# Kernel tuning notes

Hardware: AMD Instinct MI355X
Metric: run time of the kernel (lower is better)

## Reference

```python
import jax, jax.numpy as jnp
import numpy as np

N_HEADS = 16
N_EMBD = 1024
HEAD_SIZE = N_EMBD // N_HEADS
B, T = 4, 2048
EPS = 1e-5


def _layernorm(x, g, b):
    mu = jnp.mean(x, axis=-1, keepdims=True)
    var = jnp.mean((x - mu) ** 2, axis=-1, keepdims=True)
    return (x - mu) * jax.lax.rsqrt(var + EPS) * g + b


def setup_inputs() -> dict:
    key = jax.random.key(0)
    ks = jax.random.split(key, 12)
    s_in = 1.0 / np.sqrt(N_EMBD)
    s_ff = 1.0 / np.sqrt(4 * N_EMBD)
    return {
        "x": jax.random.normal(ks[0], (B, T, N_EMBD), jnp.float32),
        "Wq": jax.random.normal(ks[1], (N_HEADS, N_EMBD, HEAD_SIZE), jnp.float32) * s_in,
        "Wk": jax.random.normal(ks[2], (N_HEADS, N_EMBD, HEAD_SIZE), jnp.float32) * s_in,
        "Wv": jax.random.normal(ks[3], (N_HEADS, N_EMBD, HEAD_SIZE), jnp.float32) * s_in,
        "Wproj": jax.random.normal(ks[4], (N_EMBD, N_EMBD), jnp.float32) * s_in,
        "bproj": jnp.zeros((N_EMBD,), jnp.float32),
        "ln1_g": jnp.ones((N_EMBD,), jnp.float32),
        "ln1_b": jnp.zeros((N_EMBD,), jnp.float32),
        "ln2_g": jnp.ones((N_EMBD,), jnp.float32),
        "ln2_b": jnp.zeros((N_EMBD,), jnp.float32),
        "W1": jax.random.normal(ks[5], (N_EMBD, 4 * N_EMBD), jnp.float32) * s_in,
        "b1": jnp.zeros((4 * N_EMBD,), jnp.float32),
        "W2": jax.random.normal(ks[6], (4 * N_EMBD, N_EMBD), jnp.float32) * s_ff,
        "b2": jnp.zeros((N_EMBD,), jnp.float32),
    }


def reference(x, Wq, Wk, Wv, Wproj, bproj, ln1_g, ln1_b, ln2_g, ln2_b, W1, b1, W2, b2):
    Bx, Tx, C = x.shape
    # --- self-attention on ln1(x) ---
    h = _layernorm(x, ln1_g, ln1_b)
    q = jnp.einsum('btc,hcd->bhtd', h, Wq)
    k = jnp.einsum('btc,hcd->bhtd', h, Wk)
    v = jnp.einsum('btc,hcd->bhtd', h, Wv)
    # NOTE: original scales by C**-0.5 where C = n_embd (full dim), not head_size
    scores = jnp.einsum('bhtd,bhsd->bhts', q, k) * (C ** -0.5)
    causal = jnp.tril(jnp.ones((Tx, Tx), dtype=bool))
    scores = jnp.where(causal, scores, -jnp.inf)
    wei = jax.nn.softmax(scores, axis=-1)
    attn = jnp.einsum('bhts,bhsd->bhtd', wei, v)  # [B,H,T,hs]
    attn = attn.transpose(0, 2, 1, 3).reshape(Bx, Tx, -1)  # concat heads -> [B,T,C]
    x = x + attn @ Wproj + bproj
    # --- feed-forward on ln2(x) ---
    h2 = _layernorm(x, ln2_g, ln2_b)
    ff = jax.nn.relu(h2 @ W1 + b1) @ W2 + b2
    return x + ff
```

## Files before the change

kernel.cpp:

```cpp
#include <hip/hip_runtime.h>
#include <math.h>

typedef short bf16x8 __attribute__((ext_vector_type(8)));
typedef float f32x4 __attribute__((ext_vector_type(4)));
typedef unsigned short u16;

__device__ __forceinline__ u16 f2bf(float f) {
    union { float f; unsigned u; } v; v.f = f;
    unsigned r = v.u + 0x7fffu + ((v.u >> 16) & 1u);
    return (u16)(r >> 16);
}

__device__ __forceinline__ void gload_lds16(const void* g, void* l) {
    __builtin_amdgcn_global_load_lds((const __attribute__((address_space(1))) void*)g,
                                     (__attribute__((address_space(3))) void*)l, 16, 0, 0);
}

__global__ __launch_bounds__(256)
void transpose_cvt(const float* __restrict__ in, u16* __restrict__ out, int R, int C)
{
    __shared__ float tile[64][65];
    const size_t slab = (size_t)blockIdx.z * R * C;
    const float* ip = in + slab;
    u16* op = out + slab;
    const int r0 = blockIdx.y * 64, c0 = blockIdx.x * 64;
    const int t = threadIdx.x;
    const int tr = t >> 6, tc = t & 63;
    #pragma unroll
    for (int i = 0; i < 16; ++i)
        tile[tr + i*4][tc] = ip[(size_t)(r0 + tr + i*4)*C + c0 + tc];
    __syncthreads();
    #pragma unroll
    for (int i = 0; i < 16; ++i)
        op[(size_t)(c0 + tr + i*4)*R + r0 + tc] = f2bf(tile[tc][tr + i*4]);
}

__global__ __launch_bounds__(256)
void ln_kernel(const float* __restrict__ x, const float* __restrict__ g,
               const float* __restrict__ b, u16* __restrict__ out)
{
    const int row = blockIdx.x;
    const int t = threadIdx.x;
    const float4 v = ((const float4*)(x + (size_t)row*1024))[t];
    float s = v.x + v.y + v.z + v.w;
    float ss = v.x*v.x + v.y*v.y + v.z*v.z + v.w*v.w;
    #pragma unroll
    for (int m = 1; m < 64; m <<= 1) {
        s  += __shfl_xor(s, m);
        ss += __shfl_xor(ss, m);
    }
    __shared__ float red[8];
    const int wave = t >> 6;
    if ((t & 63) == 0) { red[wave] = s; red[4 + wave] = ss; }
    __syncthreads();
    s  = red[0] + red[1] + red[2] + red[3];
    ss = red[4] + red[5] + red[6] + red[7];
    const float mu = s * (1.f/1024.f);
    const float rs = rsqrtf(ss * (1.f/1024.f) - mu*mu + 1e-5f);
    const float4 gv = ((const float4*)g)[t];
    const float4 bv = ((const float4*)b)[t];
    ushort4 ov;
    ov.x = f2bf((v.x - mu)*rs*gv.x + bv.x);
    ov.y = f2bf((v.y - mu)*rs*gv.y + bv.y);
    ov.z = f2bf((v.z - mu)*rs*gv.z + bv.z);
    ov.w = f2bf((v.w - mu)*rs*gv.w + bv.w);
    ((ushort4*)(out + (size_t)row*1024))[t] = ov;
}

template<int NWG, int BN, int N, int K, int EPI>
__global__ __launch_bounds__(512, 2)
void gemm256_kernel(const u16* __restrict__ A, const u16* __restrict__ BT,
                    float* __restrict__ out_f32, u16* __restrict__ out_bf16,
                    const float* __restrict__ bias, const float* __restrict__ res,
                    u16* __restrict__ qbuf, u16* __restrict__ kbuf, u16* __restrict__ vt)
{
    constexpr int NI  = BN / 128;
    constexpr int NCB = BN / 64;
    __shared__ u16 As[2][256*64];
    __shared__ u16 Bs[2][BN*64];

    const int bid = blockIdx.x;
    const int tid = ((bid & 7) * (NWG / 8)) + (bid >> 3);
    const int m0 = (tid & 31) * 256;
    const int n0 = (tid >> 5) * BN;
    const int t = threadIdx.x;
    const int lane = t & 63;
    const int l15 = lane & 15, lg = lane >> 4;
    const int wid = t >> 6;
    const int wm = wid >> 2, wn = wid & 3;
    const int swzf = (l15 & 7) << 4;

    f32x4 acc[2][2][4][NI] = {};
    bf16x8 af[4][2], b0[NI][2], b1[NI][2];

    const int srow = t >> 3;
    const int sg8  = ((t & 7) ^ (srow & 7)) * 8;

#define SA_H(BUF, K0, H) do { \
    _Pragma("unroll") \
    for (int i = 2*(H); i < 2*(H)+2; ++i) \
        gload_lds16(A + (size_t)(m0 + i*64 + srow)*K + (K0) + sg8, &As[BUF][i*4096 + t*8]); \
} while (0)
#define SB_H(BUF, K0, H) do { \
    _Pragma("unroll") \
    for (int i = (NCB/2)*(H); i < (NCB/2)*(H) + NCB/2; ++i) \
        gload_lds16(BT + (size_t)(n0 + i*64 + srow)*K + (K0) + sg8, &Bs[BUF][i*4096 + t*8]); \
} while (0)
#define RD_A(CUR, QM) do { \
    _Pragma("unroll") \
    for (int mi = 0; mi < 4; ++mi) \
        _Pragma("unroll") \
        for (int kk = 0; kk < 2; ++kk) \
            af[mi][kk] = *(const bf16x8*)((const char*)&As[CUR][0] \
                + ((QM)*128 + wm*64 + mi*16 + l15)*128 + ((kk*64 + lg*16) ^ swzf)); \
} while (0)
#define RD_B(CUR, QN, DST) do { \
    _Pragma("unroll") \
    for (int ni = 0; ni < NI; ++ni) \
        _Pragma("unroll") \
        for (int kk = 0; kk < 2; ++kk) \
            DST[ni][kk] = *(const bf16x8*)((const char*)&Bs[CUR][0] \
                + ((QN)*(BN/2) + wn*(BN/8) + ni*16 + l15)*128 + ((kk*64 + lg*16) ^ swzf)); \
} while (0)
#define MFMAQ(QM, QN, BF) do { \
    _Pragma("unroll") \
    for (int mi = 0; mi < 4; ++mi) \
        _Pragma("unroll") \
        for (int ni = 0; ni < NI; ++ni) \
            _Pragma("unroll") \
            for (int kk = 0; kk < 2; ++kk) \
                acc[QM][QN][mi][ni] = __builtin_amdgcn_mfma_f32_16x16x32_bf16( \
                    af[mi][kk], BF[ni][kk], acc[QM][QN][mi][ni], 0, 0, 0); \
} while (0)
#define PH_MFMA(QM, QN, BF) do { \
    __builtin_amdgcn_sched_barrier(0); \
    __builtin_amdgcn_s_barrier(); \
    asm volatile("s_waitcnt lgkmcnt(0)" ::: "memory"); \
    __builtin_amdgcn_sched_barrier(0); \
    __builtin_amdgcn_s_setprio(1); \
    MFMAQ(QM, QN, BF); \
    __builtin_amdgcn_s_setprio(0); \
    __builtin_amdgcn_sched_barrier(0); \
} while (0)
#define BAR __builtin_amdgcn_s_barrier()
#define W_B1S do { if constexpr (BN == 256) asm volatile("s_waitcnt vmcnt(6)":::"memory"); \
                   else                     asm volatile("s_waitcnt vmcnt(5)":::"memory"); } while (0)
#define W_A1S do { if constexpr (BN == 256) asm volatile("s_waitcnt vmcnt(6)":::"memory"); \
                   else                     asm volatile("s_waitcnt vmcnt(4)":::"memory"); } while (0)
#define W_01S do { if constexpr (BN == 256) asm volatile("s_waitcnt vmcnt(4)":::"memory"); \
                   else                     asm volatile("s_waitcnt vmcnt(3)":::"memory"); } while (0)
#define W_B1L asm volatile("s_waitcnt vmcnt(2)":::"memory")
#define W_A1L asm volatile("s_waitcnt vmcnt(0)":::"memory")

    SA_H(0, 0, 0); SB_H(0, 0, 0);
    SB_H(0, 0, 1);
    SA_H(0, 0, 1);
    W_01S; BAR;

    const int NKT = K / 64;
    for (int kt = 0; kt < NKT - 1; ++kt) {
        const int cur = kt & 1, nxt = cur ^ 1;
        const int k1 = (kt + 1) * 64;
        RD_A(cur, 0); RD_B(cur, 0, b0);
        SA_H(nxt, k1, 0); SB_H(nxt, k1, 0);
        PH_MFMA(0, 0, b0);
        W_B1S; BAR;
        RD_B(cur, 1, b1);
        SB_H(nxt, k1, 1);
        PH_MFMA(0, 1, b1);
        W_A1S; BAR;
        RD_A(cur, 1);
        SA_H(nxt, k1, 1);
        PH_MFMA(1, 1, b1);
        BAR;
        PH_MFMA(1, 0, b0);
        W_01S; BAR;
    }
    {
        const int cur = (NKT - 1) & 1;
        RD_A(cur, 0); RD_B(cur, 0, b0);
        PH_MFMA(0, 0, b0);
        W_B1L; BAR;
        RD_B(cur, 1, b1);
        PH_MFMA(0, 1, b1);
        W_A1L; BAR;
        RD_A(cur, 1);
        PH_MFMA(1, 1, b1);
        BAR;
        PH_MFMA(1, 0, b0);
    }
#undef SA_H
#undef SB_H
#undef RD_A
#undef RD_B
#undef MFMAQ
#undef PH_MFMA
#undef BAR
#undef W_B1S
#undef W_A1S
#undef W_01S
#undef W_B1L
#undef W_A1L

    #pragma unroll
    for (int qm = 0; qm < 2; ++qm)
      #pragma unroll
      for (int qn = 0; qn < 2; ++qn)
        #pragma unroll
        for (int mi = 0; mi < 4; ++mi)
          #pragma unroll
          for (int ni = 0; ni < NI; ++ni) {
            const int gc = n0 + qn*(BN/2) + wn*(BN/8) + ni*16 + l15;
            #pragma unroll
            for (int j = 0; j < 4; ++j) {
                const int gr = m0 + qm*128 + wm*64 + mi*16 + lg*4 + j;
                float v = acc[qm][qn][mi][ni][j];
                if constexpr (EPI == 0) {
                    u16 bv = f2bf(v);
                    if (gc < 1024) {
                        qbuf[(size_t)gr*1024 + gc] = bv;
                    } else if (gc < 2048) {
                        kbuf[(size_t)gr*1024 + (gc - 1024)] = bv;
                    } else {
                        const int hd = gc - 2048;
                        const int bb = gr >> 11, tt = gr & 2047;
                        vt[(size_t)((bb*16 + (hd >> 6))*64 + (hd & 63))*2048 + tt] = bv;
                    }
                } else if constexpr (EPI == 1) {
                    out_f32[(size_t)gr*N + gc] = v + bias[gc] + res[(size_t)gr*N + gc];
                } else {
                    out_bf16[(size_t)gr*N + gc] = f2bf(fmaxf(v + bias[gc], 0.f));
                }
            }
          }
}

__device__ __forceinline__ void attn_qtile(
    bf16x8 (&qf)[2][2], f32x4 (&o)[2][4], float (&mprev)[2][4], float (&lsum)[2][4],
    const u16* Ksc, const u16* Vsc, u16* pl,
    int key0, int q0, int l15, int lg, int swzf, int swzp)
{
    #pragma unroll
    for (int mi = 0; mi < 2; ++mi) {
        if (key0 > q0 + mi*16 + 15) continue;
        f32x4 s[4] = {};
        #pragma unroll
        for (int n = 0; n < 4; ++n)
            #pragma unroll
            for (int kk = 0; kk < 2; ++kk) {
                const int row = n*16 + l15;
                bf16x8 kf = *(const bf16x8*)((const char*)Ksc
                                + row*128 + ((kk*64 + lg*16) ^ swzf));
                s[n] = __builtin_amdgcn_mfma_f32_16x16x32_bf16(qf[mi][kk], kf, s[n], 0, 0, 0);
            }
        const bool domask = (key0 + 63) > (q0 + mi*16);
        float tm[4] = {-INFINITY, -INFINITY, -INFINITY, -INFINITY};
        #pragma unroll
        for (int n = 0; n < 4; ++n)
            #pragma unroll
            for (int j = 0; j < 4; ++j) {
                float sv = s[n][j] * 0.03125f;
                if (domask && (key0 + n*16 + l15 > q0 + mi*16 + lg*4 + j)) sv = -INFINITY;
                s[n][j] = sv;
                tm[j] = fmaxf(tm[j], sv);
            }
        #pragma unroll
        for (int m = 1; m < 16; m <<= 1)
            #pragma unroll
            for (int j = 0; j < 4; ++j)
                tm[j] = fmaxf(tm[j], __shfl_xor(tm[j], m, 16));
        float alpha[4], rsum[4];
        #pragma unroll
        for (int j = 0; j < 4; ++j) {
            float mn = fmaxf(mprev[mi][j], tm[j]);
            alpha[j] = __expf(mprev[mi][j] - mn);
            mprev[mi][j] = mn;
            rsum[j] = 0.f;
        }
        #pragma unroll
        for (int n = 0; n < 4; ++n)
            #pragma unroll
            for (int j = 0; j < 4; ++j) {
                float pv = __expf(s[n][j] - mprev[mi][j]);
                rsum[j] += pv;
                const int qq = lg*4 + j;
                pl[qq*64 + ((n*16 + l15) ^ ((qq & 7) * 8))] = f2bf(pv);
            }
        #pragma unroll
        for (int m = 1; m < 16; m <<= 1)
            #pragma unroll
            for (int j = 0; j < 4; ++j)
                rsum[j] += __shfl_xor(rsum[j], m, 16);
        #pragma unroll
        for (int j = 0; j < 4; ++j)
            lsum[mi][j] = lsum[mi][j]*alpha[j] + rsum[j];
        #pragma unroll
        for (int dn = 0; dn < 4; ++dn)
            #pragma unroll
            for (int j = 0; j < 4; ++j)
                o[mi][dn][j] *= alpha[j];
        bf16x8 pf[2];
        #pragma unroll
        for (int kk = 0; kk < 2; ++kk)
            pf[kk] = *(const bf16x8*)(pl + l15*64 + ((kk*32 + lg*8) ^ swzp));
        #pragma unroll
        for (int dn = 0; dn < 4; ++dn)
            #pragma unroll
            for (int kk = 0; kk < 2; ++kk) {
                const int row = dn*16 + l15;
                bf16x8 vf = *(const bf16x8*)((const char*)Vsc
                                + row*128 + ((kk*64 + lg*16) ^ swzf));
                o[mi][dn] = __builtin_amdgcn_mfma_f32_16x16x32_bf16(pf[kk], vf, o[mi][dn], 0, 0, 0);
            }
    }
}

__global__ __launch_bounds__(256, 2)
void attn_kernel(const u16* __restrict__ q, const u16* __restrict__ k,
                 const u16* __restrict__ vt, u16* __restrict__ out)
{
    __shared__ u16 Ks[2][4096];
    __shared__ u16 Vs[2][4096];
    __shared__ u16 Plds[4][1024];

    const int bh = blockIdx.x & 63;
    const int pair = blockIdx.x >> 6;
    const int b = bh >> 4, h = bh & 15;
    const int wave = threadIdx.x >> 6, lane = threadIdx.x & 63;
    const int l15 = lane & 15, lg = lane >> 4;
    const int qA = pair, qB = 15 - pair;
    const int q0A = qA*128 + wave*32;
    const int q0B = qB*128 + wave*32;
    const u16* Qp = q + (size_t)b*2048*1024 + h*64;
    const u16* Kp = k + (size_t)b*2048*1024 + h*64;
    const u16* Vp = vt + (size_t)bh*64*2048;
    u16* pl = Plds[wave];

    bf16x8 qfA[2][2], qfB[2][2];
    #pragma unroll
    for (int mi = 0; mi < 2; ++mi)
        #pragma unroll
        for (int kk = 0; kk < 2; ++kk) {
            qfA[mi][kk] = *(const bf16x8*)(Qp + (size_t)(q0A + mi*16 + l15)*1024 + kk*32 + lg*8);
            qfB[mi][kk] = *(const bf16x8*)(Qp + (size_t)(q0B + mi*16 + l15)*1024 + kk*32 + lg*8);
        }

    const int srow0 = wave*8 + (lane >> 3);
    const int scol  = ((lane & 7) ^ (srow0 & 7)) << 3;
    const int swzf  = (l15 & 7) << 4;
    const int swzp  = (l15 & 7) << 3;

    f32x4 oA[2][4] = {}, oB[2][4] = {};
    float mprevA[2][4], lsumA[2][4], mprevB[2][4], lsumB[2][4];
    #pragma unroll
    for (int mi = 0; mi < 2; ++mi)
        #pragma unroll
        for (int j = 0; j < 4; ++j) {
            mprevA[mi][j] = -INFINITY; lsumA[mi][j] = 0.f;
            mprevB[mi][j] = -INFINITY; lsumB[mi][j] = 0.f;
        }

    const int nkt = 32 - 2*pair;

    #define STAGE(buf, key0_) do { \
        gload_lds16(Kp + (size_t)((key0_) + srow0)*1024 + scol,      &Ks[buf][wave*512]); \
        gload_lds16(Kp + (size_t)((key0_) + srow0 + 32)*1024 + scol, &Ks[buf][(4+wave)*512]); \
        gload_lds16(Vp + (size_t)srow0*2048 + (key0_) + scol,        &Vs[buf][wave*512]); \
        gload_lds16(Vp + (size_t)(srow0+32)*2048 + (key0_) + scol,   &Vs[buf][(4+wave)*512]); \
    } while (0)

    STAGE(0, 0);

    for (int kt = 0; kt < nkt; ++kt) {
        const int cur = kt & 1;
        const int key0 = kt * 64;
        if (kt + 1 < nkt) {
            STAGE(cur ^ 1, key0 + 64);
            asm volatile("s_waitcnt vmcnt(4)" ::: "memory");
        } else {
            asm volatile("s_waitcnt vmcnt(0)" ::: "memory");
        }
        __builtin_amdgcn_s_barrier();
        __builtin_amdgcn_sched_barrier(0);

        if (key0 <= q0A + 31)
            attn_qtile(qfA, oA, mprevA, lsumA, &Ks[cur][0], &Vs[cur][0], pl,
                       key0, q0A, l15, lg, swzf, swzp);
        if (key0 <= q0B + 31)
            attn_qtile(qfB, oB, mprevB, lsumB, &Ks[cur][0], &Vs[cur][0], pl,
                       key0, q0B, l15, lg, swzf, swzp);

        __builtin_amdgcn_sched_barrier(0);
        __builtin_amdgcn_s_barrier();
    }
    #undef STAGE

    #pragma unroll
    for (int mi = 0; mi < 2; ++mi)
        #pragma unroll
        for (int dn = 0; dn < 4; ++dn)
            #pragma unroll
            for (int j = 0; j < 4; ++j) {
                float vA = oA[mi][dn][j] / lsumA[mi][j];
                out[(size_t)(b*2048 + q0A + mi*16 + lg*4 + j)*1024 + h*64 + dn*16 + l15] = f2bf(vA);
                float vB = oB[mi][dn][j] / lsumB[mi][j];
                out[(size_t)(b*2048 + q0B + mi*16 + lg*4 + j)*1024 + h*64 + dn*16 + l15] = f2bf(vB);
            }
}

#define MB(x) ((size_t)(x) << 20)

extern "C" void kernel_launch(void* const* d_in, const int* in_sizes, int n_in,
                              void* d_out, int out_size, void* d_ws, size_t ws_size,
                              hipStream_t stream) {
    const float* x      = (const float*)d_in[0];
    const float* Wq     = (const float*)d_in[1];
    const float* Wk     = (const float*)d_in[2];
    const float* Wv     = (const float*)d_in[3];
    const float* Wproj  = (const float*)d_in[4];
    const float* bproj  = (const float*)d_in[5];
    const float* ln1_g  = (const float*)d_in[6];
    const float* ln1_b  = (const float*)d_in[7];
    const float* ln2_g  = (const float*)d_in[8];
    const float* ln2_b  = (const float*)d_in[9];
    const float* W1     = (const float*)d_in[10];
    const float* b1     = (const float*)d_in[11];
    const float* W2     = (const float*)d_in[12];
    const float* b2     = (const float*)d_in[13];
    float* out = (float*)d_out;

    char* ws = (char*)d_ws;
    u16*  h      = (u16*)(ws + MB(0));
    u16*  qbuf   = (u16*)(ws + MB(16));
    u16*  kbuf   = (u16*)(ws + MB(32));
    u16*  vt     = (u16*)(ws + MB(48));
    u16*  attn   = (u16*)(ws + MB(64));
    float* x2    = (float*)(ws + MB(80));
    u16*  BTqkv  = (u16*)(ws + MB(112));
    u16*  BTproj = (u16*)(ws + MB(118));
    u16*  BT1    = (u16*)(ws + MB(120));
    u16*  BT2    = (u16*)(ws + MB(128));
    u16*  ff     = (u16*)(ws + MB(16));
    u16*  h2     = h;

    transpose_cvt<<<dim3(1,16,16),  256, 0, stream>>>(Wq,    BTqkv,             1024, 64);
    transpose_cvt<<<dim3(1,16,16),  256, 0, stream>>>(Wk,    BTqkv + (1<<20),   1024, 64);
    transpose_cvt<<<dim3(1,16,16),  256, 0, stream>>>(Wv,    BTqkv + (2<<20),   1024, 64);
    transpose_cvt<<<dim3(16,16,1),  256, 0, stream>>>(Wproj, BTproj,            1024, 1024);
    transpose_cvt<<<dim3(64,16,1),  256, 0, stream>>>(W1,    BT1,               1024, 4096);
    transpose_cvt<<<dim3(16,64,1),  256, 0, stream>>>(W2,    BT2,               4096, 1024);

    ln_kernel<<<8192, 256, 0, stream>>>(x, ln1_g, ln1_b, h);
    gemm256_kernel<384,256,3072,1024,0><<<384, 512, 0, stream>>>(h, BTqkv, nullptr, nullptr,
        nullptr, nullptr, qbuf, kbuf, vt);
    attn_kernel<<<512, 256, 0, stream>>>(qbuf, kbuf, vt, attn);
    gemm256_kernel<256,128,1024,1024,1><<<256, 512, 0, stream>>>(attn, BTproj, x2, nullptr,
        bproj, x, nullptr, nullptr, nullptr);
    ln_kernel<<<8192, 256, 0, stream>>>(x2, ln2_g, ln2_b, h2);
    gemm256_kernel<512,256,4096,1024,2><<<512, 512, 0, stream>>>(h2, BT1, nullptr, ff,
        b1, nullptr, nullptr, nullptr, nullptr);
    gemm256_kernel<256,128,1024,4096,1><<<256, 512, 0, stream>>>(ff, BT2, out, nullptr,
        b2, x2, nullptr, nullptr, nullptr);
}
```

Before: 603.5 us.

## Deepen GEMM global-to-LDS prefetch to two k-tiles ahead with half-buffer reuse

Restructures the GEMM main loop so global-to-LDS loads for tile kt+2 are issued into the current buffer's halves as soon as each half has been read into registers. Only one wait remains per iteration, at steady state, instead of a wait at each phase. The aim is to hide global memory latency behind more MFMA work. Correctness now depends on subtle LDS half-buffer reuse ordering across barriers, and two peeled tail iterations are added.

Result: slower. 652.9 us (+8.2%).

```diff
diff --git a/kernel.cpp b/kernel.cpp
--- a/kernel.cpp
+++ b/kernel.cpp
@@ -143,50 +143,50 @@
     __builtin_amdgcn_sched_barrier(0); \
 } while (0)
 #define BAR __builtin_amdgcn_s_barrier()
-#define W_B1S do { if constexpr (BN == 256) asm volatile("s_waitcnt vmcnt(6)":::"memory"); \
-                   else                     asm volatile("s_waitcnt vmcnt(5)":::"memory"); } while (0)
-#define W_A1S do { if constexpr (BN == 256) asm volatile("s_waitcnt vmcnt(6)":::"memory"); \
-                   else                     asm volatile("s_waitcnt vmcnt(4)":::"memory"); } while (0)
-#define W_01S do { if constexpr (BN == 256) asm volatile("s_waitcnt vmcnt(4)":::"memory"); \
-                   else                     asm volatile("s_waitcnt vmcnt(3)":::"memory"); } while (0)
-#define W_B1L asm volatile("s_waitcnt vmcnt(2)":::"memory")
-#define W_A1L asm volatile("s_waitcnt vmcnt(0)":::"memory")
-
-    SA_H(0, 0, 0); SB_H(0, 0, 0);
-    SB_H(0, 0, 1);
-    SA_H(0, 0, 1);
-    W_01S; BAR;
+#define W_STEADY do { if constexpr (BN == 256) asm volatile("s_waitcnt vmcnt(6)":::"memory"); \
+                      else                     asm volatile("s_waitcnt vmcnt(4)":::"memory"); } while (0)
+
+    SA_H(0, 0, 0); SB_H(0, 0, 0); SB_H(0, 0, 1); SA_H(0, 0, 1);
+    SA_H(1, 64, 0); SB_H(1, 64, 0); SB_H(1, 64, 1);
+    W_STEADY; BAR;
 
     const int NKT = K / 64;
-    for (int kt = 0; kt < NKT - 1; ++kt) {
+    for (int kt = 0; kt < NKT - 2; ++kt) {
         const int cur = kt & 1, nxt = cur ^ 1;
-        const int k1 = (kt + 1) * 64;
+        const int k1 = (kt + 1) * 64, k2 = (kt + 2) * 64;
         RD_A(cur, 0); RD_B(cur, 0, b0);
-        SA_H(nxt, k1, 0); SB_H(nxt, k1, 0);
-        PH_MFMA(0, 0, b0);
-        W_B1S; BAR;
+        SA_H(nxt, k1, 1);
+        PH_MFMA(0, 0, b0); BAR;
         RD_B(cur, 1, b1);
-        SB_H(nxt, k1, 1);
-        PH_MFMA(0, 1, b1);
-        W_A1S; BAR;
+        SA_H(cur, k2, 0);
+        PH_MFMA(0, 1, b1); BAR;
         RD_A(cur, 1);
-        SA_H(nxt, k1, 1);
-        PH_MFMA(1, 1, b1);
-        BAR;
+        SB_H(cur, k2, 0);
+        PH_MFMA(1, 1, b1); BAR;
+        SB_H(cur, k2, 1);
         PH_MFMA(1, 0, b0);
-        W_01S; BAR;
+        W_STEADY; BAR;
+    }
+    {
+        const int cur = (NKT - 2) & 1, nxt = cur ^ 1;
+        RD_A(cur, 0); RD_B(cur, 0, b0);
+        SA_H(nxt, (NKT - 1) * 64, 1);
+        PH_MFMA(0, 0, b0); BAR;
+        RD_B(cur, 1, b1);
+        PH_MFMA(0, 1, b1); BAR;
+        RD_A(cur, 1);
+        PH_MFMA(1, 1, b1); BAR;
+        PH_MFMA(1, 0, b0);
+        asm volatile("s_waitcnt vmcnt(0)" ::: "memory"); BAR;
     }
     {
         const int cur = (NKT - 1) & 1;
         RD_A(cur, 0); RD_B(cur, 0, b0);
-        PH_MFMA(0, 0, b0);
-        W_B1L; BAR;
+        PH_MFMA(0, 0, b0); BAR;
         RD_B(cur, 1, b1);
-        PH_MFMA(0, 1, b1);
-        W_A1L; BAR;
+        PH_MFMA(0, 1, b1); BAR;
         RD_A(cur, 1);
-        PH_MFMA(1, 1, b1);
-        BAR;
+        PH_MFMA(1, 1, b1); BAR;
         PH_MFMA(1, 0, b0);
     }
 #undef SA_H
@@ -196,11 +196,7 @@
 #undef MFMAQ
 #undef PH_MFMA
 #undef BAR
-#undef W_B1S
-#undef W_A1S
-#undef W_01S
-#undef W_B1L
-#undef W_A1L
+#undef W_STEADY
 
     #pragma unroll
     for (int qm = 0; qm < 2; ++qm)
```

## Halve attention query tile per block, double grid, fold softmax scale into Q

Applied to the files above, without the earlier changes.

Attention blocks now process 64-row query tiles (16 rows per wave) paired from opposite ends of the causal triangle, doubling the grid to 1024 blocks and raising the occupancy hint to 4 blocks per CU. The 1/32 score scale is folded into the Q projection epilogue, removing a multiply per score element. This aims to improve load balance and latency hiding through more resident waves. The cost is that each K/V tile is reused across fewer queries, so K/V global traffic roughly doubles, and rounding Q to bf16 after scaling by a power of two leaves the numerics unchanged.

After: 641.8 us. 1.06x slower.

```diff
diff --git a/kernel.cpp b/kernel.cpp
--- a/kernel.cpp
+++ b/kernel.cpp
@@ -216,15 +216,14 @@
                 const int gr = m0 + qm*128 + wm*64 + mi*16 + lg*4 + j;
                 float v = acc[qm][qn][mi][ni][j];
                 if constexpr (EPI == 0) {
-                    u16 bv = f2bf(v);
                     if (gc < 1024) {
-                        qbuf[(size_t)gr*1024 + gc] = bv;
+                        qbuf[(size_t)gr*1024 + gc] = f2bf(v * 0.03125f);
                     } else if (gc < 2048) {
-                        kbuf[(size_t)gr*1024 + (gc - 1024)] = bv;
+                        kbuf[(size_t)gr*1024 + (gc - 1024)] = f2bf(v);
                     } else {
                         const int hd = gc - 2048;
                         const int bb = gr >> 11, tt = gr & 2047;
-                        vt[(size_t)((bb*16 + (hd >> 6))*64 + (hd & 63))*2048 + tt] = bv;
+                        vt[(size_t)((bb*16 + (hd >> 6))*64 + (hd & 63))*2048 + tt] = f2bf(v);
                     }
                 } else if constexpr (EPI == 1) {
                     out_f32[(size_t)gr*N + gc] = v + bias[gc] + res[(size_t)gr*N + gc];
@@ -235,87 +234,83 @@
           }
 }
 
-__device__ __forceinline__ void attn_qtile(
-    bf16x8 (&qf)[2][2], f32x4 (&o)[2][4], float (&mprev)[2][4], float (&lsum)[2][4],
+__device__ __forceinline__ void attn_qtile1(
+    bf16x8 (&qf)[2], f32x4 (&o)[4], float (&mprev)[4], float (&lsum)[4],
     const u16* Ksc, const u16* Vsc, u16* pl,
     int key0, int q0, int l15, int lg, int swzf, int swzp)
 {
-    #pragma unroll
-    for (int mi = 0; mi < 2; ++mi) {
-        if (key0 > q0 + mi*16 + 15) continue;
-        f32x4 s[4] = {};
-        #pragma unroll
-        for (int n = 0; n < 4; ++n)
-            #pragma unroll
-            for (int kk = 0; kk < 2; ++kk) {
-                const int row = n*16 + l15;
-                bf16x8 kf = *(const bf16x8*)((const char*)Ksc
-                                + row*128 + ((kk*64 + lg*16) ^ swzf));
-                s[n] = __builtin_amdgcn_mfma_f32_16x16x32_bf16(qf[mi][kk], kf, s[n], 0, 0, 0);
-            }
-        const bool domask = (key0 + 63) > (q0 + mi*16);
-        float tm[4] = {-INFINITY, -INFINITY, -INFINITY, -INFINITY};
-        #pragma unroll
-        for (int n = 0; n < 4; ++n)
-            #pragma unroll
-            for (int j = 0; j < 4; ++j) {
-                float sv = s[n][j] * 0.03125f;
-                if (domask && (key0 + n*16 + l15 > q0 + mi*16 + lg*4 + j)) sv = -INFINITY;
-                s[n][j] = sv;
-                tm[j] = fmaxf(tm[j], sv);
-            }
-        #pragma unroll
-        for (int m = 1; m < 16; m <<= 1)
-            #pragma unroll
-            for (int j = 0; j < 4; ++j)
-                tm[j] = fmaxf(tm[j], __shfl_xor(tm[j], m, 16));
-        float alpha[4], rsum[4];
+    f32x4 s[4] = {};
+    #pragma unroll
+    for (int n = 0; n < 4; ++n)
+        #pragma unroll
+        for (int kk = 0; kk < 2; ++kk) {
+            const int row = n*16 + l15;
+            bf16x8 kf = *(const bf16x8*)((const char*)Ksc
+                            + row*128 + ((kk*64 + lg*16) ^ swzf));
+            s[n] = __builtin_amdgcn_mfma_f32_16x16x32_bf16(qf[kk], kf, s[n], 0, 0, 0);
+        }
+    const bool domask = (key0 + 63) > q0;
+    float tm[4] = {-INFINITY, -INFINITY, -INFINITY, -INFINITY};
+    #pragma unroll
+    for (int n = 0; n < 4; ++n)
         #pragma unroll
         for (int j = 0; j < 4; ++j) {
-            float mn = fmaxf(mprev[mi][j], tm[j]);
-            alpha[j] = __expf(mprev[mi][j] - mn);
-            mprev[mi][j] = mn;
-            rsum[j] = 0.f;
-        }
-        #pragma unroll
-        for (int n = 0; n < 4; ++n)
-            #pragma unroll
-            for (int j = 0; j < 4; ++j) {
-                float pv = __expf(s[n][j] - mprev[mi][j]);
-                rsum[j] += pv;
-                const int qq = lg*4 + j;
-                pl[qq*64 + ((n*16 + l15) ^ ((qq & 7) * 8))] = f2bf(pv);
-            }
-        #pragma unroll
-        for (int m = 1; m < 16; m <<= 1)
-            #pragma unroll
-            for (int j = 0; j < 4; ++j)
-                rsum[j] += __shfl_xor(rsum[j], m, 16);
+            float sv = s[n][j];
+            if (domask && (key0 + n*16 + l15 > q0 + lg*4 + j)) sv = -INFINITY;
+            s[n][j] = sv;
+            tm[j] = fmaxf(tm[j], sv);
+        }
+    #pragma unroll
+    for (int m = 1; m < 16; m <<= 1)
         #pragma unroll
         for (int j = 0; j < 4; ++j)
-            lsum[mi][j] = lsum[mi][j]*alpha[j] + rsum[j];
-        #pragma unroll
-        for (int dn = 0; dn < 4; ++dn)
-            #pragma unroll
-            for (int j = 0; j < 4; ++j)
-                o[mi][dn][j] *= alpha[j];
-        bf16x8 pf[2];
-        #pragma unroll
-        for (int kk = 0; kk < 2; ++kk)
-            pf[kk] = *(const bf16x8*)(pl + l15*64 + ((kk*32 + lg*8) ^ swzp));
-        #pragma unroll
-        for (int dn = 0; dn < 4; ++dn)
-            #pragma unroll
-            for (int kk = 0; kk < 2; ++kk) {
-                const int row = dn*16 + l15;
-                bf16x8 vf = *(const bf16x8*)((const char*)Vsc
-                                + row*128 + ((kk*64 + lg*16) ^ swzf));
-                o[mi][dn] = __builtin_amdgcn_mfma_f32_16x16x32_bf16(pf[kk], vf, o[mi][dn], 0, 0, 0);
-            }
-    }
-}
-
-__global__ __launch_bounds__(256, 2)
+            tm[j] = fmaxf(tm[j], __shfl_xor(tm[j], m, 16));
+    float alpha[4], rsum[4];
+    #pragma unroll
+    for (int j = 0; j < 4; ++j) {
+        float mn = fmaxf(mprev[j], tm[j]);
+        alpha[j] = __expf(mprev[j] - mn);
+        mprev[j] = mn;
+        rsum[j] = 0.f;
+    }
+    #pragma unroll
+    for (int n = 0; n < 4; ++n)
+        #pragma unroll
+        for (int j = 0; j < 4; ++j) {
+            float pv = __expf(s[n][j] - mprev[j]);
+            rsum[j] += pv;
+            const int qq = lg*4 + j;
+            pl[qq*64 + ((n*16 + l15) ^ ((qq & 7) * 8))] = f2bf(pv);
+        }
+    #pragma unroll
+    for (int m = 1; m < 16; m <<= 1)
+        #pragma unroll
+        for (int j = 0; j < 4; ++j)
+            rsum[j] += __shfl_xor(rsum[j], m, 16);
+    #pragma unroll
+    for (int j = 0; j < 4; ++j)
+        lsum[j] = lsum[j]*alpha[j] + rsum[j];
+    #pragma unroll
+    for (int dn = 0; dn < 4; ++dn)
+        #pragma unroll
+        for (int j = 0; j < 4; ++j)
+            o[dn][j] *= alpha[j];
+    bf16x8 pf[2];
+    #pragma unroll
+    for (int kk = 0; kk < 2; ++kk)
+        pf[kk] = *(const bf16x8*)(pl + l15*64 + ((kk*32 + lg*8) ^ swzp));
+    #pragma unroll
+    for (int dn = 0; dn < 4; ++dn)
+        #pragma unroll
+        for (int kk = 0; kk < 2; ++kk) {
+            const int row = dn*16 + l15;
+            bf16x8 vf = *(const bf16x8*)((const char*)Vsc
+                            + row*128 + ((kk*64 + lg*16) ^ swzf));
+            o[dn] = __builtin_amdgcn_mfma_f32_16x16x32_bf16(pf[kk], vf, o[dn], 0, 0, 0);
+        }
+}
+
+__global__ __launch_bounds__(256, 4)
 void attn_kernel(const u16* __restrict__ q, const u16* __restrict__ k,
                  const u16* __restrict__ vt, u16* __restrict__ out)
 {
@@ -328,39 +323,34 @@
     const int b = bh >> 4, h = bh & 15;
     const int wave = threadIdx.x >> 6, lane = threadIdx.x & 63;
     const int l15 = lane & 15, lg = lane >> 4;
-    const int qA = pair, qB = 15 - pair;
-    const int q0A = qA*128 + wave*32;
-    const int q0B = qB*128 + wave*32;
+    const int q0A = pair*64 + wave*16;
+    const int q0B = (31 - pair)*64 + wave*16;
     const u16* Qp = q + (size_t)b*2048*1024 + h*64;
     const u16* Kp = k + (size_t)b*2048*1024 + h*64;
     const u16* Vp = vt + (size_t)bh*64*2048;
     u16* pl = Plds[wave];
 
-    bf16x8 qfA[2][2], qfB[2][2];
-    #pragma unroll
-    for (int mi = 0; mi < 2; ++mi)
-        #pragma unroll
-        for (int kk = 0; kk < 2; ++kk) {
-            qfA[mi][kk] = *(const bf16x8*)(Qp + (size_t)(q0A + mi*16 + l15)*1024 + kk*32 + lg*8);
-            qfB[mi][kk] = *(const bf16x8*)(Qp + (size_t)(q0B + mi*16 + l15)*1024 + kk*32 + lg*8);
-        }
+    bf16x8 qfA[2], qfB[2];
+    #pragma unroll
+    for (int kk = 0; kk < 2; ++kk) {
+        qfA[kk] = *(const bf16x8*)(Qp + (size_t)(q0A + l15)*1024 + kk*32 + lg*8);
+        qfB[kk] = *(const bf16x8*)(Qp + (size_t)(q0B + l15)*1024 + kk*32 + lg*8);
+    }
 
     const int srow0 = wave*8 + (lane >> 3);
     const int scol  = ((lane & 7) ^ (srow0 & 7)) << 3;
     const int swzf  = (l15 & 7) << 4;
     const int swzp  = (l15 & 7) << 3;
 
-    f32x4 oA[2][4] = {}, oB[2][4] = {};
-    float mprevA[2][4], lsumA[2][4], mprevB[2][4], lsumB[2][4];
-    #pragma unroll
-    for (int mi = 0; mi < 2; ++mi)
-        #pragma unroll
-        for (int j = 0; j < 4; ++j) {
-            mprevA[mi][j] = -INFINITY; lsumA[mi][j] = 0.f;
-            mprevB[mi][j] = -INFINITY; lsumB[mi][j] = 0.f;
-        }
-
-    const int nkt = 32 - 2*pair;
+    f32x4 oA[4] = {}, oB[4] = {};
+    float mprevA[4], lsumA[4], mprevB[4], lsumB[4];
+    #pragma unroll
+    for (int j = 0; j < 4; ++j) {
+        mprevA[j] = -INFINITY; lsumA[j] = 0.f;
+        mprevB[j] = -INFINITY; lsumB[j] = 0.f;
+    }
+
+    const int nkt = 32 - pair;
 
     #define STAGE(buf, key0_) do { \
         gload_lds16(Kp + (size_t)((key0_) + srow0)*1024 + scol,      &Ks[buf][wave*512]); \
@@ -383,12 +373,11 @@
         __builtin_amdgcn_s_barrier();
         __builtin_amdgcn_sched_barrier(0);
 
-        if (key0 <= q0A + 31)
-            attn_qtile(qfA, oA, mprevA, lsumA, &Ks[cur][0], &Vs[cur][0], pl,
-                       key0, q0A, l15, lg, swzf, swzp);
-        if (key0 <= q0B + 31)
-            attn_qtile(qfB, oB, mprevB, lsumB, &Ks[cur][0], &Vs[cur][0], pl,
-                       key0, q0B, l15, lg, swzf, swzp);
+        if (kt <= pair)
+            attn_qtile1(qfA, oA, mprevA, lsumA, &Ks[cur][0], &Vs[cur][0], pl,
+                        key0, q0A, l15, lg, swzf, swzp);
+        attn_qtile1(qfB, oB, mprevB, lsumB, &Ks[cur][0], &Vs[cur][0], pl,
+                    key0, q0B, l15, lg, swzf, swzp);
 
         __builtin_amdgcn_sched_barrier(0);
         __builtin_amdgcn_s_barrier();
@@ -396,16 +385,14 @@
     #undef STAGE
 
     #pragma unroll
-    for (int mi = 0; mi < 2; ++mi)
-        #pragma unroll
-        for (int dn = 0; dn < 4; ++dn)
-            #pragma unroll
-            for (int j = 0; j < 4; ++j) {
-                float vA = oA[mi][dn][j] / lsumA[mi][j];
-                out[(size_t)(b*2048 + q0A + mi*16 + lg*4 + j)*1024 + h*64 + dn*16 + l15] = f2bf(vA);
-                float vB = oB[mi][dn][j] / lsumB[mi][j];
-                out[(size_t)(b*2048 + q0B + mi*16 + lg*4 + j)*1024 + h*64 + dn*16 + l15] = f2bf(vB);
-            }
+    for (int dn = 0; dn < 4; ++dn)
+        #pragma unroll
+        for (int j = 0; j < 4; ++j) {
+            float vA = oA[dn][j] / lsumA[j];
+            out[(size_t)(b*2048 + q0A + lg*4 + j)*1024 + h*64 + dn*16 + l15] = f2bf(vA);
+            float vB = oB[dn][j] / lsumB[j];
+            out[(size_t)(b*2048 + q0B + lg*4 + j)*1024 + h*64 + dn*16 + l15] = f2bf(vB);
+        }
 }
 
 #define MB(x) ((size_t)(x) << 20)
@@ -453,7 +440,7 @@
     ln_kernel<<<8192, 256, 0, stream>>>(x, ln1_g, ln1_b, h);
     gemm256_kernel<384,256,3072,1024,0><<<384, 512, 0, stream>>>(h, BTqkv, nullptr, nullptr,
         nullptr, nullptr, qbuf, kbuf, vt);
-    attn_kernel<<<512, 256, 0, stream>>>(qbuf, kbuf, vt, attn);
+    attn_kernel<<<1024, 256, 0, stream>>>(qbuf, kbuf, vt, attn);
     gemm256_kernel<256,128,1024,1024,1><<<256, 512, 0, stream>>>(attn, BTproj, x2, nullptr,
         bproj, x, nullptr, nullptr, nullptr);
     ln_kernel<<<8192, 256, 0, stream>>>(x2, ln2_g, ln2_b, h2);
```
